# Kernel optimization log

Hardware: AMD Instinct MI355X
Metric: run time of the kernel (lower is better)

## Reference

```python
import jax, jax.numpy as jnp
import numpy as np

B, T, C, H, W, NC = 128, 32, 512, 8, 32, 6625
HH = C // 2  # per-direction LSTM hidden


def setup_inputs() -> dict:
    key = jax.random.key(0)
    ks = jax.random.split(key, 20)
    u = lambda k, shape, n: jax.random.uniform(k, shape, jnp.float32, -1.0 / np.sqrt(n), 1.0 / np.sqrt(n))
    return dict(
        feature=jax.random.normal(ks[0], (B, C, H, W), jnp.float32),
        attention_map=jax.random.uniform(ks[1], (B, T, H, W), jnp.float32) + 1e-3,
        text=jax.random.randint(ks[2], (B, T), 0, NC),
        text_length=jnp.full((B,), T, dtype=jnp.int32),
        char_embeddings=jax.random.normal(ks[3], (NC, C), jnp.float32),
        lstm_w_ih_f=u(ks[4], (4 * HH, C), HH),
        lstm_w_hh_f=u(ks[5], (4 * HH, HH), HH),
        lstm_b_ih_f=u(ks[6], (4 * HH,), HH),
        lstm_b_hh_f=u(ks[7], (4 * HH,), HH),
        lstm_w_ih_b=u(ks[8], (4 * HH, C), HH),
        lstm_w_hh_b=u(ks[9], (4 * HH, HH), HH),
        lstm_b_ih_b=u(ks[10], (4 * HH,), HH),
        lstm_b_hh_b=u(ks[11], (4 * HH,), HH),
        gru_w_ih=u(ks[12], (3 * C, 2 * C), C),
        gru_w_hh=u(ks[13], (3 * C, C), C),
        gru_b_ih=u(ks[14], (3 * C,), C),
        gru_b_hh=u(ks[15], (3 * C,), C),
        gen_w=u(ks[16], (NC, C), C),
        gen_b=u(ks[17], (NC,), C),
    )


def _lstm_dir(xs, w_ih, w_hh, b_ih, b_hh):
    # xs: [T, B, C] -> hs: [T, B, HH]; PyTorch gate order i, f, g, o
    b = xs.shape[1]
    hh = w_hh.shape[1]
    def step(carry, xt):
        h, c = carry
        g = xt @ w_ih.T + h @ w_hh.T + (b_ih + b_hh)
        i, f, gg, o = jnp.split(g, 4, axis=-1)
        c = jax.nn.sigmoid(f) * c + jax.nn.sigmoid(i) * jnp.tanh(gg)
        h = jax.nn.sigmoid(o) * jnp.tanh(c)
        return (h, c), h
    h0 = jnp.zeros((b, hh), xs.dtype)
    _, hs = jax.lax.scan(step, (h0, h0), xs)
    return hs


def reference(feature, attention_map, text, text_length, char_embeddings,
              lstm_w_ih_f, lstm_w_hh_f, lstm_b_ih_f, lstm_b_hh_f,
              lstm_w_ih_b, lstm_w_hh_b, lstm_b_ih_b, lstm_b_hh_b,
              gru_w_ih, gru_w_hh, gru_b_ih, gru_b_hh, gen_w, gen_b):
    b, c, h, w = feature.shape
    t = attention_map.shape[1]
    # normalize attention over spatial dims, attention-pool features: [T, B, C]
    att = attention_map / attention_map.sum(axis=(2, 3), keepdims=True)
    cseq = jnp.einsum('bchw,bthw->tbc', feature, att)
    # bidirectional LSTM (dropout is identity in eval mode)
    hs_f = _lstm_dir(cseq, lstm_w_ih_f, lstm_w_hh_f, lstm_b_ih_f, lstm_b_hh_f)
    hs_b = _lstm_dir(cseq[::-1], lstm_w_ih_b, lstm_w_hh_b, lstm_b_ih_b, lstm_b_hh_b)[::-1]
    cseq = jnp.concatenate([hs_f, hs_b], axis=-1)  # [T, B, C]
    # teacher-forced previous-char embeddings: step 0 uses index 0
    prev_idx = jnp.concatenate([jnp.zeros((b, 1), text.dtype), text[:, :-1]], axis=1)  # [B, T]
    prev_emb = jnp.transpose(char_embeddings[prev_idx], (1, 0, 2))  # [T, B, C]
    # GRUCell decode; PyTorch gate order r, z, n
    def gru_step(hid, inp):
        ct, pe = inp
        x = jnp.concatenate([ct, pe], axis=-1)  # [B, 2C]
        gi = x @ gru_w_ih.T + gru_b_ih
        gh = hid @ gru_w_hh.T + gru_b_hh
        ir, iz, inn = jnp.split(gi, 3, axis=-1)
        hr, hz, hn = jnp.split(gh, 3, axis=-1)
        r = jax.nn.sigmoid(ir + hr)
        z = jax.nn.sigmoid(iz + hz)
        n = jnp.tanh(inn + r * hn)
        hid = (1.0 - z) * n + z * hid
        return hid, hid
    h0 = jnp.zeros((b, c), cseq.dtype)
    _, gru_res = jax.lax.scan(gru_step, h0, (cseq, prev_emb))  # [T, B, C]
    logits = gru_res @ gen_w.T + gen_b  # [T, B, NC]
    # pack per text_length; lengths are all == T so this equals a reshape
    out_res = jnp.transpose(logits, (1, 0, 2)).reshape(b * t, -1)
    out_attentions = att.reshape(b * t, h, w)
    return (out_res, out_attentions)
```

## Files before the change

### kernel.cpp

```cpp
#include <hip/hip_runtime.h>
#include <math.h>

typedef __attribute__((ext_vector_type(8))) short sh8;
typedef __attribute__((ext_vector_type(4))) short sh4;
typedef __attribute__((ext_vector_type(4))) float f4;
typedef __attribute__((ext_vector_type(4))) unsigned u4;

__device__ inline short f2bf(float f) {
    union { float f; unsigned u; } v; v.f = f;
    unsigned u = v.u;
    return (short)((u + 0x7fffu + ((u >> 16) & 1u)) >> 16);
}
__device__ inline sh8 as_sh8(u4 v) { union { u4 u; sh8 s; } c; c.u = v; return c.s; }

__device__ inline float sigm(float x)  { return __builtin_amdgcn_rcpf(1.f + __builtin_amdgcn_exp2f(-1.44269504f * x)); }
__device__ inline float tanha(float x) { return 1.f - 2.f * __builtin_amdgcn_rcpf(1.f + __builtin_amdgcn_exp2f(2.88539008f * x)); }

__device__ inline sh8 frag8(const float* __restrict__ p) {
    f4 a = *(const f4*)p;
    f4 b = *(const f4*)(p + 4);
    sh8 r;
    r[0]=f2bf(a[0]); r[1]=f2bf(a[1]); r[2]=f2bf(a[2]); r[3]=f2bf(a[3]);
    r[4]=f2bf(b[0]); r[5]=f2bf(b[1]); r[6]=f2bf(b[2]); r[7]=f2bf(b[3]);
    return r;
}

__device__ inline u4 cload_u4(const void* p) {
    u4 r;
    asm volatile("global_load_dwordx4 %0, %1, off sc0 sc1" : "=v"(r) : "v"(p));
    return r;
}

__device__ inline void grp_signal(int* myflag, int epoch) {
    asm volatile("s_waitcnt vmcnt(0)" ::: "memory");
    __builtin_amdgcn_sched_barrier(0);
    __syncthreads();
    if (threadIdx.x == 0)
        __hip_atomic_store(myflag, epoch, __ATOMIC_RELAXED, __HIP_MEMORY_SCOPE_AGENT);
}
__device__ inline void grp_wait(const int* fbase, int nb, int epoch) {
    if (threadIdx.x < 64) {
        int lane = threadIdx.x;
        bool need = lane < nb;
        const int* fp = fbase + lane * 16;
        while (true) {
            int v = need ? __hip_atomic_load(fp, __ATOMIC_RELAXED, __HIP_MEMORY_SCOPE_AGENT)
                         : 0x7fffffff;
            if (__ballot(need && (v < epoch)) == 0ull) break;
            __builtin_amdgcn_s_sleep(1);
        }
    }
    __syncthreads();
}
__device__ inline void prefetch_drain() {
    asm volatile("s_waitcnt vmcnt(0)" ::: "memory");
    __builtin_amdgcn_sched_barrier(0);
}

__global__ void zero_ctr(int* c, int n) {
    int i = blockIdx.x * blockDim.x + threadIdx.x;
    if (i < n) c[i] = 0;
}

struct CvtPack { const float* s[7]; short* d[7]; int n4[7]; };
__global__ void cvt_bf16(CvtPack p) {
    int job = blockIdx.y;
    const f4* s = (const f4*)p.s[job];
    sh4* d = (sh4*)p.d[job];
    int n4 = p.n4[job];
    for (int i = blockIdx.x * blockDim.x + threadIdx.x; i < n4; i += gridDim.x * blockDim.x) {
        f4 v = s[i];
        sh4 o; o[0]=f2bf(v[0]); o[1]=f2bf(v[1]); o[2]=f2bf(v[2]); o[3]=f2bf(v[3]);
        d[i] = o;
    }
}

__global__ void bias_prep(const float* bihf, const float* bhhf,
                          const float* bihb, const float* bhhb, float* biasL) {
    int n = blockIdx.x * blockDim.x + threadIdx.x;
    biasL[n] = (n < 1024) ? bihf[n] + bhhf[n] : bihb[n - 1024] + bhhb[n - 1024];
}

__global__ void att_norm(const float* __restrict__ att, float* __restrict__ outA) {
    int row = blockIdx.x;
    int tid = threadIdx.x;
    const float* p = att + (size_t)row * 256;
    f4 v = *(const f4*)(p + tid * 4);
    float sum = v[0] + v[1] + v[2] + v[3];
    #pragma unroll
    for (int off = 32; off; off >>= 1) sum += __shfl_down(sum, off);
    float inv = 1.f / __shfl(sum, 0);
    f4 o; o[0]=v[0]*inv; o[1]=v[1]*inv; o[2]=v[2]*inv; o[3]=v[3]*inv;
    *(f4*)(outA + (size_t)row * 256 + tid * 4) = o;
}

__global__ __launch_bounds__(256)
void pool_gemm(const float* __restrict__ feature, const float* __restrict__ att,
               short* __restrict__ cseqb) {
    int bz = blockIdx.y;
    const float* A  = feature + (size_t)bz * 512 * 256;
    const float* Wt = att + (size_t)bz * 32 * 256;
    int wave = threadIdx.x >> 6, lane = threadIdx.x & 63, r = lane & 15, hh = lane >> 4;
    int m0 = blockIdx.x * 64 + wave * 16;
    f4 acc[2] = {};
    const float* ar = A  + (size_t)(m0 + r) * 256 + hh * 8;
    const float* w0 = Wt + (size_t)r * 256 + hh * 8;
    const float* w1 = Wt + (size_t)(16 + r) * 256 + hh * 8;
    for (int kk = 0; kk < 256; kk += 32) {
        sh8 af = frag8(ar + kk);
        acc[0] = __builtin_amdgcn_mfma_f32_16x16x32_bf16(af, frag8(w0 + kk), acc[0], 0, 0, 0);
        acc[1] = __builtin_amdgcn_mfma_f32_16x16x32_bf16(af, frag8(w1 + kk), acc[1], 0, 0, 0);
    }
    #pragma unroll
    for (int j = 0; j < 2; j++) {
        int t = j * 16 + r;
        #pragma unroll
        for (int reg = 0; reg < 4; reg++) {
            int c = m0 + hh * 4 + reg;
            cseqb[(size_t)t * 65536 + (size_t)bz * 512 + c] = f2bf(acc[j][reg]);
        }
    }
}

template<int MODE>
__global__ __launch_bounds__(256)
void gemm128(const short* __restrict__ A, const short* __restrict__ W,
             const float* __restrict__ bias1, const float* __restrict__ bias2,
             float* __restrict__ out, int M, int N, int K) {
    __shared__ short lds[2][2][4096];
    const int tid = threadIdx.x, wave = tid >> 6, lane = tid & 63;
    const int r = lane & 15, hh = lane >> 4;
    const int wm = wave >> 1, wn = wave & 1;

    int bx = blockIdx.x, by = blockIdx.y;
    {
        int gx = gridDim.x;
        int nwg = gx * gridDim.y;
        if ((nwg & 7) == 0) {
            int id = by * gx + bx;
            int cpx = nwg >> 3;
            int swz = (id & 7) * cpx + (id >> 3);
            bx = swz % gx;
            by = swz / gx;
        }
    }
    const int m0 = bx * 128, n0 = by * 128;

    const int c0 = tid, c1 = 256 + tid;
    const int r0 = c0 >> 2, r1 = c1 >> 2;
    const int s0 = ((c0 & 3) ^ ((r0 >> 1) & 3));
    const int s1 = ((c1 & 3) ^ ((r1 >> 1) & 3));
    const short* gA0 = A + (size_t)(m0 + r0) * K + s0 * 8;
    const short* gA1 = A + (size_t)(m0 + r1) * K + s1 * 8;
    int wr0 = n0 + r0; if (wr0 > N - 1) wr0 = N - 1;
    int wr1 = n0 + r1; if (wr1 > N - 1) wr1 = N - 1;
    const short* gW0 = W + (size_t)wr0 * K + s0 * 8;
    const short* gW1 = W + (size_t)wr1 * K + s1 * 8;
    const int lo0 = (wave * 64) * 8, lo1 = (256 + wave * 64) * 8;

    auto stage = [&](int buf, int kt) {
        int ko = kt * 32;
        __builtin_amdgcn_global_load_lds((const __attribute__((address_space(1))) void*)(gA0 + ko),
            (__attribute__((address_space(3))) void*)&lds[buf][0][lo0], 16, 0, 0);
        __builtin_amdgcn_global_load_lds((const __attribute__((address_space(1))) void*)(gA1 + ko),
            (__attribute__((address_space(3))) void*)&lds[buf][0][lo1], 16, 0, 0);
        __builtin_amdgcn_global_load_lds((const __attribute__((address_space(1))) void*)(gW0 + ko),
            (__attribute__((address_space(3))) void*)&lds[buf][1][lo0], 16, 0, 0);
        __builtin_amdgcn_global_load_lds((const __attribute__((address_space(1))) void*)(gW1 + ko),
            (__attribute__((address_space(3))) void*)&lds[buf][1][lo1], 16, 0, 0);
    };

    f4 acc[4][4] = {};
    const int NT = K / 32;
    int cur = 0;

    stage(0, 0);
    __syncthreads();
    for (int kt = 0; kt < NT; ++kt) {
        if (kt + 1 < NT) stage(cur ^ 1, kt + 1);
        const char* As = (const char*)&lds[cur][0][0];
        const char* Ws = (const char*)&lds[cur][1][0];
        sh8 a[4], b[4];
        #pragma unroll
        for (int i = 0; i < 4; i++) {
            int row = wm * 64 + i * 16 + r;
            a[i] = *(const sh8*)(As + row * 64 + ((hh ^ ((row >> 1) & 3)) * 16));
        }
        #pragma unroll
        for (int i = 0; i < 4; i++) {
            int row = wn * 64 + i * 16 + r;
            b[i] = *(const sh8*)(Ws + row * 64 + ((hh ^ ((row >> 1) & 3)) * 16));
        }
        #pragma unroll
        for (int i = 0; i < 4; i++)
            #pragma unroll
            for (int j = 0; j < 4; j++)
                acc[i][j] = __builtin_amdgcn_mfma_f32_16x16x32_bf16(a[i], b[j], acc[i][j], 0, 0, 0);
        __syncthreads();
        cur ^= 1;
    }

    float bsj[4];
    #pragma unroll
    for (int j = 0; j < 4; j++) {
        int n = n0 + wn * 64 + j * 16 + r;
        int nc = n < N ? n : N - 1;
        bsj[j] = (bias1 ? bias1[nc] : 0.f) + (bias2 ? bias2[nc] : 0.f);
    }

    float* fl = (float*)&lds[0][0][0];
    #pragma unroll
    for (int hhalf = 0; hhalf < 2; hhalf++) {
        __syncthreads();
        if (wm == hhalf) {
            #pragma unroll
            for (int i = 0; i < 4; i++)
                #pragma unroll
                for (int j = 0; j < 4; j++) {
                    int col = wn * 64 + j * 16 + r;
                    #pragma unroll
                    for (int reg = 0; reg < 4; reg++)
                        fl[(i * 16 + hh * 4 + reg) * 128 + col] = acc[i][j][reg] + bsj[j];
                }
        }
        __syncthreads();
        #pragma unroll
        for (int it = 0; it < 8; it++) {
            int c = it * 256 + tid;
            int row = c >> 5, cf4 = c & 31;
            int n = n0 + cf4 * 4;
            int mrow = m0 + hhalf * 64 + row;
            size_t orow = (MODE == 0) ? (size_t)mrow
                                      : ((size_t)(mrow & 127) * 32 + (mrow >> 7));
            if (n + 3 < N) {
                *(f4*)&out[orow * N + n] = *(const f4*)&fl[row * 128 + cf4 * 4];
            } else {
                #pragma unroll
                for (int d = 0; d < 4; d++)
                    if (n + d < N) out[orow * N + n + d] = fl[row * 128 + cf4 * 4 + d];
            }
        }
    }
}

__global__ void emb_fill(const int* __restrict__ text, const float* __restrict__ emb,
                         short* __restrict__ xcatb) {
    int n = blockIdx.x;
    int t = n >> 7, b = n & 127;
    int idx = (t == 0) ? 0 : text[b * 32 + (t - 1)];
    const f4* src = (const f4*)(emb + (size_t)idx * 512);
    sh4* dst = (sh4*)(xcatb + (size_t)n * 1024 + 512);
    for (int j = threadIdx.x; j < 128; j += 64) {
        f4 v = src[j];
        sh4 o; o[0]=f2bf(v[0]); o[1]=f2bf(v[1]); o[2]=f2bf(v[2]); o[3]=f2bf(v[3]);
        dst[j] = o;
    }
}

__global__ __launch_bounds__(128)
void lstm_chain(const float* __restrict__ xfb,
                const short* __restrict__ whhf_b, const short* __restrict__ whhb_b,
                short* __restrict__ xcatb,
                int* __restrict__ flags) {
    __shared__ short wlds[64 * 256];
    const int blk = blockIdx.x;
    const int dir = blk >> 6;
    const int mg  = (blk >> 4) & 3;
    const int ug  = blk & 15;
    const int m0 = mg * 32, u0 = ug * 16;
    const short* whh = dir ? whhb_b : whhf_b;
    const int dcol = dir ? 256 : 0;

    int* grp_flags = flags + (dir * 4 + mg) * 16 * 16;
    int* my_flag   = grp_flags + ug * 16;

    const int tid = threadIdx.x, mt = tid >> 6, lane = tid & 63;
    const int r = lane & 15, hh = lane >> 4;
    unsigned* xcat32 = (unsigned*)xcatb;

    for (int i = 0; i < 16; i++) {
        int c = i * 128 + tid;
        int col = c >> 5, off = c & 31;
        int g = col >> 4, ul = col & 15;
        sh8 v = *(const sh8*)(whh + ((size_t)(g * 256 + u0 + ul)) * 256 + off * 8);
        *(sh8*)((char*)wlds + col * 512 + ((off * 16) ^ ((col & 7) << 4))) = v;
    }
    __syncthreads();

    const int arow_m = m0 + mt * 16 + r;
    const int u = u0 + r;
    const int mb = m0 + mt * 16 + hh * 4;
    float c_state[4] = {0.f, 0.f, 0.f, 0.f};

    float xv[4][4];
    {
        const int t0 = dir ? 31 : 0;
        #pragma unroll
        for (int g = 0; g < 4; g++)
            #pragma unroll
            for (int reg = 0; reg < 4; reg++)
                xv[g][reg] = xfb[((size_t)t0 * 128 + mb + reg) * 2048 + dir * 1024 + g * 256 + u];
    }

    for (int s = 0; s < 32; s++) {
        const int t = dir ? (31 - s) : s;
        f4 acc[4] = {};
        if (s > 0) {
            grp_wait(grp_flags, 16, s);
            const int tp = dir ? (t + 1) : (t - 1);
            const short* arow = xcatb + ((size_t)tp * 128 + arow_m) * 1024 + dcol + hh * 8;
            u4 afr[8];
            #pragma unroll
            for (int kk = 0; kk < 8; kk++) afr[kk] = cload_u4(arow + kk * 32);
            asm volatile("s_waitcnt vmcnt(0)" ::: "memory");
            __builtin_amdgcn_sched_barrier(0);
            #pragma unroll
            for (int kk = 0; kk < 8; kk++) {
                sh8 af = as_sh8(afr[kk]);
                #pragma unroll
                for (int g = 0; g < 4; g++) {
                    int colr = g * 16 + r;
                    sh8 bf = *(const sh8*)((const char*)wlds + colr * 512 +
                              (((kk * 64 + hh * 16)) ^ ((colr & 7) << 4)));
                    acc[g] = __builtin_amdgcn_mfma_f32_16x16x32_bf16(af, bf, acc[g], 0, 0, 0);
                }
            }
        }
        #pragma unroll
        for (int reg = 0; reg < 4; reg++) {
            int m = mb + reg;
            float gI = acc[0][reg] + xv[0][reg];
            float gF = acc[1][reg] + xv[1][reg];
            float gG = acc[2][reg] + xv[2][reg];
            float gO = acc[3][reg] + xv[3][reg];
            float cn = sigm(gF) * c_state[reg] + sigm(gI) * tanha(gG);
            c_state[reg] = cn;
            float h = sigm(gO) * tanha(cn);
            unsigned hb = (unsigned)(unsigned short)f2bf(h);
            unsigned pb = (unsigned)__shfl_xor((int)hb, 1, 64);
            if (!(r & 1))
                __hip_atomic_store(&xcat32[((size_t)t * 128 + m) * 512 + ((dcol + u) >> 1)],
                                   hb | (pb << 16), __ATOMIC_RELAXED, __HIP_MEMORY_SCOPE_AGENT);
        }
        if (s < 31) {
            grp_signal(my_flag, s + 1);
            const int tn = dir ? (t - 1) : (t + 1);
            #pragma unroll
            for (int g = 0; g < 4; g++)
                #pragma unroll
                for (int reg = 0; reg < 4; reg++)
                    xv[g][reg] = xfb[((size_t)tn * 128 + mb + reg) * 2048 + dir * 1024 + g * 256 + u];
            prefetch_drain();
        }
    }
}

__global__ __launch_bounds__(128)
void gru_chain(const float* __restrict__ gi,
               const short* __restrict__ gwhh_b, const float* __restrict__ bhh,
               short* __restrict__ gresb,
               int* __restrict__ flags) {
    extern __shared__ short wlds[];
    const int blk = blockIdx.x;
    const int mg = blk >> 4, ug = blk & 15;
    const int m0 = mg * 16, u0 = ug * 32;

    int* grp_flags = flags + mg * 16 * 16;
    int* my_flag   = grp_flags + ug * 16;

    const int tid = threadIdx.x, w = tid >> 6, lane = tid & 63;
    const int r = lane & 15, hh = lane >> 4;
    unsigned* gres32 = (unsigned*)gresb;

    for (int i = 0; i < 48; i++) {
        int c = i * 128 + tid;
        int col = c >> 6, off = c & 63;
        int g = col >> 5, ul = col & 31;
        sh8 v = *(const sh8*)(gwhh_b + ((size_t)(g * 512 + u0 + ul)) * 512 + off * 8);
        *(sh8*)((char*)wlds + col * 1024 + ((off * 16) ^ ((col & 7) << 4))) = v;
    }
    __syncthreads();

    const int mb = m0 + hh * 4;
    const int u = u0 + w * 16 + r;
    const float bh_r = bhh[u], bh_z = bhh[512 + u], bh_n = bhh[1024 + u];
    float h_state[4] = {0.f, 0.f, 0.f, 0.f};

    float gv[3][4];
    #pragma unroll
    for (int g = 0; g < 3; g++)
        #pragma unroll
        for (int reg = 0; reg < 4; reg++)
            gv[g][reg] = gi[((size_t)(mb + reg)) * 1536 + g * 512 + u];

    for (int t = 0; t < 32; t++) {
        f4 acc[3] = {};
        if (t > 0) {
            grp_wait(grp_flags, 16, t);
            const short* arow = gresb + ((size_t)(t - 1) * 128 + m0 + r) * 512 + hh * 8;
            u4 afr[16];
            #pragma unroll
            for (int kk = 0; kk < 16; kk++) afr[kk] = cload_u4(arow + kk * 32);
            asm volatile("s_waitcnt vmcnt(0)" ::: "memory");
            __builtin_amdgcn_sched_barrier(0);
            #pragma unroll
            for (int kk = 0; kk < 16; kk++) {
                sh8 af = as_sh8(afr[kk]);
                #pragma unroll
                for (int g = 0; g < 3; g++) {
                    int colr = g * 32 + w * 16 + r;
                    sh8 bf = *(const sh8*)((const char*)wlds + colr * 1024 +
                              ((kk * 64 + hh * 16) ^ ((colr & 7) << 4)));
                    acc[g] = __builtin_amdgcn_mfma_f32_16x16x32_bf16(af, bf, acc[g], 0, 0, 0);
                }
            }
        }
        #pragma unroll
        for (int reg = 0; reg < 4; reg++) {
            int m = mb + reg;
            float rr = sigm(gv[0][reg] + acc[0][reg] + bh_r);
            float zz = sigm(gv[1][reg] + acc[1][reg] + bh_z);
            float nn = tanha(gv[2][reg] + rr * (acc[2][reg] + bh_n));
            float h = (1.f - zz) * nn + zz * h_state[reg];
            h_state[reg] = h;
            unsigned hb = (unsigned)(unsigned short)f2bf(h);
            unsigned pb = (unsigned)__shfl_xor((int)hb, 1, 64);
            if (!(r & 1))
                __hip_atomic_store(&gres32[((size_t)t * 128 + m) * 256 + (u >> 1)],
                                   hb | (pb << 16), __ATOMIC_RELAXED, __HIP_MEMORY_SCOPE_AGENT);
        }
        if (t < 31) {
            grp_signal(my_flag, t + 1);
            #pragma unroll
            for (int g = 0; g < 3; g++)
                #pragma unroll
                for (int reg = 0; reg < 4; reg++)
                    gv[g][reg] = gi[((size_t)(t + 1) * 128 + mb + reg) * 1536 + g * 512 + u];
            prefetch_drain();
        }
    }
}

extern "C" void kernel_launch(void* const* d_in, const int* in_sizes, int n_in,
                              void* d_out, int out_size, void* d_ws, size_t ws_size,
                              hipStream_t stream) {
    const float* feature = (const float*)d_in[0];
    const float* attmap  = (const float*)d_in[1];
    const int*   text    = (const int*)d_in[2];
    const float* cemb    = (const float*)d_in[4];
    const float* wihf    = (const float*)d_in[5];
    const float* whhf    = (const float*)d_in[6];
    const float* bihf    = (const float*)d_in[7];
    const float* bhhf    = (const float*)d_in[8];
    const float* wihb    = (const float*)d_in[9];
    const float* whhb    = (const float*)d_in[10];
    const float* bihb    = (const float*)d_in[11];
    const float* bhhb    = (const float*)d_in[12];
    const float* gwih    = (const float*)d_in[13];
    const float* gwhh    = (const float*)d_in[14];
    const float* gbih    = (const float*)d_in[15];
    const float* gbhh    = (const float*)d_in[16];
    const float* genw    = (const float*)d_in[17];
    const float* genb    = (const float*)d_in[18];

    float* out    = (float*)d_out;
    float* outAtt = out + (size_t)4096 * 6625;

    float* xfb   = (float*)d_ws;
    float* gi    = xfb + 8388608;
    float* biasL = gi + 6291456;
    int*   flags = (int*)(biasL + 2048);
    short* cseqb  = (short*)(flags + 4096);
    short* xcatb  = cseqb + 2097152;
    short* gresb  = xcatb + 4194304;
    short* wih_b  = gresb + 2097152;
    short* whhf_b = wih_b + 1048576;
    short* whhb_b = whhf_b + 262144;
    short* gwih_b = whhb_b + 262144;
    short* gwhh_b = gwih_b + 1572864;
    short* genw_b = gwhh_b + 786432;

    hipFuncSetAttribute((const void*)gru_chain,
                        hipFuncAttributeMaxDynamicSharedMemorySize, 98304);

    zero_ctr<<<dim3(16), dim3(256), 0, stream>>>(flags, 4096);

    CvtPack p;
    p.s[0] = wihf; p.d[0] = wih_b;           p.n4[0] = 524288 / 4;
    p.s[1] = wihb; p.d[1] = wih_b + 524288;  p.n4[1] = 524288 / 4;
    p.s[2] = whhf; p.d[2] = whhf_b;          p.n4[2] = 262144 / 4;
    p.s[3] = whhb; p.d[3] = whhb_b;          p.n4[3] = 262144 / 4;
    p.s[4] = gwih; p.d[4] = gwih_b;          p.n4[4] = 1572864 / 4;
    p.s[5] = gwhh; p.d[5] = gwhh_b;          p.n4[5] = 786432 / 4;
    p.s[6] = genw; p.d[6] = genw_b;          p.n4[6] = 3392000 / 4;
    cvt_bf16<<<dim3(128, 7), dim3(256), 0, stream>>>(p);
    bias_prep<<<dim3(8), dim3(256), 0, stream>>>(bihf, bhhf, bihb, bhhb, biasL);

    att_norm<<<dim3(4096), dim3(64), 0, stream>>>(attmap, outAtt);
    pool_gemm<<<dim3(8, 128), dim3(256), 0, stream>>>(feature, outAtt, cseqb);

    gemm128<0><<<dim3(32, 16), dim3(256), 0, stream>>>(cseqb, wih_b, biasL, nullptr,
                                                       xfb, 4096, 2048, 512);
    emb_fill<<<dim3(4096), dim3(64), 0, stream>>>(text, cemb, xcatb);

    lstm_chain<<<dim3(128), dim3(128), 0, stream>>>(xfb, whhf_b, whhb_b, xcatb, flags);

    gemm128<0><<<dim3(32, 12), dim3(256), 0, stream>>>(xcatb, gwih_b, gbih, nullptr,
                                                       gi, 4096, 1536, 1024);

    gru_chain<<<dim3(128), dim3(128), 98304, stream>>>(gi, gwhh_b, gbhh, gresb, flags + 2048);

    gemm128<1><<<dim3(32, 52), dim3(256), 0, stream>>>(gresb, genw_b, genb, nullptr,
                                                       out, 4096, 6625, 512);
}
```

Baseline: 385.0 us.

## Add 256x128 GEMM tile for generator projection and fuse prep kernels

Adds a new gemm256 kernel with 512 threads and a 256-row M tile for the final vocabulary projection. It stages A and W tiles into LDS with direct global-to-LDS loads and double buffering, so each loaded W tile is reused across twice as many rows. The zero-counter and bias-prep kernels are merged into one launch to remove a kernel launch. The cost is higher LDS and register pressure per workgroup and only 832 workgroups for the large GEMM.

```diff
diff --git a/kernel.cpp b/kernel.cpp
--- a/kernel.cpp
+++ b/kernel.cpp
@@ -57,9 +57,12 @@
     __builtin_amdgcn_sched_barrier(0);
 }
 
-__global__ void zero_ctr(int* c, int n) {
+__global__ void prep(int* flags, const float* bihf, const float* bhhf,
+                     const float* bihb, const float* bhhb, float* biasL) {
     int i = blockIdx.x * blockDim.x + threadIdx.x;
-    if (i < n) c[i] = 0;
+    flags[i] = 0;
+    if (i < 2048)
+        biasL[i] = (i < 1024) ? bihf[i] + bhhf[i] : bihb[i - 1024] + bhhb[i - 1024];
 }
 
 struct CvtPack { const float* s[7]; short* d[7]; int n4[7]; };
@@ -73,12 +76,6 @@
         sh4 o; o[0]=f2bf(v[0]); o[1]=f2bf(v[1]); o[2]=f2bf(v[2]); o[3]=f2bf(v[3]);
         d[i] = o;
     }
-}
-
-__global__ void bias_prep(const float* bihf, const float* bhhf,
-                          const float* bihb, const float* bhhb, float* biasL) {
-    int n = blockIdx.x * blockDim.x + threadIdx.x;
-    biasL[n] = (n < 1024) ? bihf[n] + bhhf[n] : bihb[n - 1024] + bhhb[n - 1024];
 }
 
 __global__ void att_norm(const float* __restrict__ att, float* __restrict__ outA) {
@@ -122,7 +119,6 @@
     }
 }
 
-template<int MODE>
 __global__ __launch_bounds__(256)
 void gemm128(const short* __restrict__ A, const short* __restrict__ W,
              const float* __restrict__ bias1, const float* __restrict__ bias2,
@@ -230,8 +226,123 @@
             int row = c >> 5, cf4 = c & 31;
             int n = n0 + cf4 * 4;
             int mrow = m0 + hhalf * 64 + row;
-            size_t orow = (MODE == 0) ? (size_t)mrow
-                                      : ((size_t)(mrow & 127) * 32 + (mrow >> 7));
+            if (n + 3 < N) {
+                *(f4*)&out[(size_t)mrow * N + n] = *(const f4*)&fl[row * 128 + cf4 * 4];
+            } else {
+                #pragma unroll
+                for (int d = 0; d < 4; d++)
+                    if (n + d < N) out[(size_t)mrow * N + n + d] = fl[row * 128 + cf4 * 4 + d];
+            }
+        }
+    }
+}
+
+__global__ __launch_bounds__(512)
+void gemm256(const short* __restrict__ A, const short* __restrict__ W,
+             const float* __restrict__ bias1,
+             float* __restrict__ out, int M, int N, int K) {
+    __shared__ short lds[2][12288];
+    const int tid = threadIdx.x, wave = tid >> 6, lane = tid & 63;
+    const int r = lane & 15, hh = lane >> 4;
+    const int wm = wave >> 1, wn = wave & 1;
+
+    int bx = blockIdx.x, by = blockIdx.y;
+    {
+        int gx = gridDim.x;
+        int nwg = gx * gridDim.y;
+        if ((nwg & 7) == 0) {
+            int id = by * gx + bx;
+            int cpx = nwg >> 3;
+            int swz = (id & 7) * cpx + (id >> 3);
+            bx = swz % gx;
+            by = swz / gx;
+        }
+    }
+    const int m0 = bx * 256, n0 = by * 128;
+
+    const int cA0 = tid, cA1 = 512 + tid, cW = tid;
+    const int rA0 = cA0 >> 2, rA1 = cA1 >> 2, rW = cW >> 2;
+    const int sA0 = (cA0 & 3) ^ ((rA0 >> 1) & 3);
+    const int sA1 = (cA1 & 3) ^ ((rA1 >> 1) & 3);
+    const int sW  = (cW & 3) ^ ((rW >> 1) & 3);
+    const short* gA0 = A + (size_t)(m0 + rA0) * K + sA0 * 8;
+    const short* gA1 = A + (size_t)(m0 + rA1) * K + sA1 * 8;
+    int wrW = n0 + rW; if (wrW > N - 1) wrW = N - 1;
+    const short* gW0 = W + (size_t)wrW * K + sW * 8;
+    const int loA0 = (wave * 64) * 8, loA1 = (512 + wave * 64) * 8;
+    const int loW  = 8192 + (wave * 64) * 8;
+
+    auto stage = [&](int buf, int kt) {
+        int ko = kt * 32;
+        __builtin_amdgcn_global_load_lds((const __attribute__((address_space(1))) void*)(gA0 + ko),
+            (__attribute__((address_space(3))) void*)&lds[buf][loA0], 16, 0, 0);
+        __builtin_amdgcn_global_load_lds((const __attribute__((address_space(1))) void*)(gA1 + ko),
+            (__attribute__((address_space(3))) void*)&lds[buf][loA1], 16, 0, 0);
+        __builtin_amdgcn_global_load_lds((const __attribute__((address_space(1))) void*)(gW0 + ko),
+            (__attribute__((address_space(3))) void*)&lds[buf][loW], 16, 0, 0);
+    };
+
+    f4 acc[4][4] = {};
+    const int NT = K / 32;
+    int cur = 0;
+
+    stage(0, 0);
+    __syncthreads();
+    for (int kt = 0; kt < NT; ++kt) {
+        if (kt + 1 < NT) stage(cur ^ 1, kt + 1);
+        const char* As = (const char*)&lds[cur][0];
+        const char* Ws = (const char*)&lds[cur][8192];
+        sh8 a[4], b[4];
+        #pragma unroll
+        for (int i = 0; i < 4; i++) {
+            int row = wm * 64 + i * 16 + r;
+            a[i] = *(const sh8*)(As + row * 64 + ((hh ^ ((row >> 1) & 3)) * 16));
+        }
+        #pragma unroll
+        for (int i = 0; i < 4; i++) {
+            int row = wn * 64 + i * 16 + r;
+            b[i] = *(const sh8*)(Ws + row * 64 + ((hh ^ ((row >> 1) & 3)) * 16));
+        }
+        #pragma unroll
+        for (int i = 0; i < 4; i++)
+            #pragma unroll
+            for (int j = 0; j < 4; j++)
+                acc[i][j] = __builtin_amdgcn_mfma_f32_16x16x32_bf16(a[i], b[j], acc[i][j], 0, 0, 0);
+        __syncthreads();
+        cur ^= 1;
+    }
+
+    float bsj[4];
+    #pragma unroll
+    for (int j = 0; j < 4; j++) {
+        int n = n0 + wn * 64 + j * 16 + r;
+        int nc = n < N ? n : N - 1;
+        bsj[j] = bias1 ? bias1[nc] : 0.f;
+    }
+
+    float* fl = (float*)&lds[0][0];
+    #pragma unroll
+    for (int q = 0; q < 4; q++) {
+        __syncthreads();
+        if (wm == q) {
+            #pragma unroll
+            for (int i = 0; i < 4; i++)
+                #pragma unroll
+                for (int j = 0; j < 4; j++) {
+                    int col = wn * 64 + j * 16 + r;
+                    #pragma unroll
+                    for (int reg = 0; reg < 4; reg++)
+                        fl[(i * 16 + hh * 4 + reg) * 128 + col] = acc[i][j][reg] + bsj[j];
+                }
+        }
+        __syncthreads();
+        #pragma unroll
+        for (int it = 0; it < 4; it++) {
+            int c = it * 512 + tid;
+            int row = c >> 5, cf4 = c & 31;
+            int n = n0 + cf4 * 4;
+            int mrow = m0 + q * 64 + row;
+            size_t orow = (size_t)(mrow & 127) * 32 + (mrow >> 7);
             if (n + 3 < N) {
                 *(f4*)&out[orow * N + n] = *(const f4*)&fl[row * 128 + cf4 * 4];
             } else {
@@ -483,7 +594,7 @@
     hipFuncSetAttribute((const void*)gru_chain,
                         hipFuncAttributeMaxDynamicSharedMemorySize, 98304);
 
-    zero_ctr<<<dim3(16), dim3(256), 0, stream>>>(flags, 4096);
+    prep<<<dim3(16), dim3(256), 0, stream>>>(flags, bihf, bhhf, bihb, bhhb, biasL);
 
     CvtPack p;
     p.s[0] = wihf; p.d[0] = wih_b;           p.n4[0] = 524288 / 4;
@@ -494,22 +605,21 @@
     p.s[5] = gwhh; p.d[5] = gwhh_b;          p.n4[5] = 786432 / 4;
     p.s[6] = genw; p.d[6] = genw_b;          p.n4[6] = 3392000 / 4;
     cvt_bf16<<<dim3(128, 7), dim3(256), 0, stream>>>(p);
-    bias_prep<<<dim3(8), dim3(256), 0, stream>>>(bihf, bhhf, bihb, bhhb, biasL);
 
     att_norm<<<dim3(4096), dim3(64), 0, stream>>>(attmap, outAtt);
     pool_gemm<<<dim3(8, 128), dim3(256), 0, stream>>>(feature, outAtt, cseqb);
 
-    gemm128<0><<<dim3(32, 16), dim3(256), 0, stream>>>(cseqb, wih_b, biasL, nullptr,
-                                                       xfb, 4096, 2048, 512);
+    gemm128<<<dim3(32, 16), dim3(256), 0, stream>>>(cseqb, wih_b, biasL, nullptr,
+                                                    xfb, 4096, 2048, 512);
     emb_fill<<<dim3(4096), dim3(64), 0, stream>>>(text, cemb, xcatb);
 
     lstm_chain<<<dim3(128), dim3(128), 0, stream>>>(xfb, whhf_b, whhb_b, xcatb, flags);
 
-    gemm128<0><<<dim3(32, 12), dim3(256), 0, stream>>>(xcatb, gwih_b, gbih, nullptr,
-                                                       gi, 4096, 1536, 1024);
+    gemm128<<<dim3(32, 12), dim3(256), 0, stream>>>(xcatb, gwih_b, gbih, nullptr,
+                                                    gi, 4096, 1536, 1024);
 
     gru_chain<<<dim3(128), dim3(128), 98304, stream>>>(gi, gwhh_b, gbhh, gresb, flags + 2048);
 
-    gemm128<1><<<dim3(32, 52), dim3(256), 0, stream>>>(gresb, genw_b, genb, nullptr,
-                                                       out, 4096, 6625, 512);
-}
+    gemm256<<<dim3(16, 52), dim3(512), 0, stream>>>(gresb, genw_b, genb,
+                                                    out, 4096, 6625, 512);
+}
```

After: 375.2 us. -2.5%, faster.

## Enlarge GEMM tile to 256x128 with 8 waves and fold bias prep into flag init

Applied to the files above, without the earlier changes.

The bf16 MFMA GEMM moves from 128x128 tiles with 4 waves to 256x128 tiles with 8 waves. Each block now stages 256 A rows and 128 W rows per k-step, so the W tile is reused across twice as many rows and fewer blocks are launched. The epilogue writes through LDS in four 64-row quarters. Separately, the bias-sum kernel is merged into the flag-zeroing kernel to save one launch. In exchange, blocks are larger and fewer, which lowers the block count for the smaller GEMMs (192 to 256 blocks), and LDS use per block rises.

```diff
diff --git a/kernel.cpp b/kernel.cpp
--- a/kernel.cpp
+++ b/kernel.cpp
@@ -57,9 +57,12 @@
     __builtin_amdgcn_sched_barrier(0);
 }
 
-__global__ void zero_ctr(int* c, int n) {
+__global__ void prep(int* flags, const float* bihf, const float* bhhf,
+                     const float* bihb, const float* bhhb, float* biasL) {
     int i = blockIdx.x * blockDim.x + threadIdx.x;
-    if (i < n) c[i] = 0;
+    flags[i] = 0;
+    if (i < 2048)
+        biasL[i] = (i < 1024) ? bihf[i] + bhhf[i] : bihb[i - 1024] + bhhb[i - 1024];
 }
 
 struct CvtPack { const float* s[7]; short* d[7]; int n4[7]; };
@@ -73,12 +76,6 @@
         sh4 o; o[0]=f2bf(v[0]); o[1]=f2bf(v[1]); o[2]=f2bf(v[2]); o[3]=f2bf(v[3]);
         d[i] = o;
     }
-}
-
-__global__ void bias_prep(const float* bihf, const float* bhhf,
-                          const float* bihb, const float* bhhb, float* biasL) {
-    int n = blockIdx.x * blockDim.x + threadIdx.x;
-    biasL[n] = (n < 1024) ? bihf[n] + bhhf[n] : bihb[n - 1024] + bhhb[n - 1024];
 }
 
 __global__ void att_norm(const float* __restrict__ att, float* __restrict__ outA) {
@@ -123,11 +120,11 @@
 }
 
 template<int MODE>
-__global__ __launch_bounds__(256)
-void gemm128(const short* __restrict__ A, const short* __restrict__ W,
-             const float* __restrict__ bias1, const float* __restrict__ bias2,
+__global__ __launch_bounds__(512)
+void gemm256(const short* __restrict__ A, const short* __restrict__ W,
+             const float* __restrict__ bias1,
              float* __restrict__ out, int M, int N, int K) {
-    __shared__ short lds[2][2][4096];
+    __shared__ short lds[2][12288];
     const int tid = threadIdx.x, wave = tid >> 6, lane = tid & 63;
     const int r = lane & 15, hh = lane >> 4;
     const int wm = wave >> 1, wn = wave & 1;
@@ -144,30 +141,28 @@
             by = swz / gx;
         }
     }
-    const int m0 = bx * 128, n0 = by * 128;
-
-    const int c0 = tid, c1 = 256 + tid;
-    const int r0 = c0 >> 2, r1 = c1 >> 2;
-    const int s0 = ((c0 & 3) ^ ((r0 >> 1) & 3));
-    const int s1 = ((c1 & 3) ^ ((r1 >> 1) & 3));
-    const short* gA0 = A + (size_t)(m0 + r0) * K + s0 * 8;
-    const short* gA1 = A + (size_t)(m0 + r1) * K + s1 * 8;
-    int wr0 = n0 + r0; if (wr0 > N - 1) wr0 = N - 1;
-    int wr1 = n0 + r1; if (wr1 > N - 1) wr1 = N - 1;
-    const short* gW0 = W + (size_t)wr0 * K + s0 * 8;
-    const short* gW1 = W + (size_t)wr1 * K + s1 * 8;
-    const int lo0 = (wave * 64) * 8, lo1 = (256 + wave * 64) * 8;
+    const int m0 = bx * 256, n0 = by * 128;
+
+    const int cA0 = tid, cA1 = 512 + tid, cW = tid;
+    const int rA0 = cA0 >> 2, rA1 = cA1 >> 2, rW = cW >> 2;
+    const int sA0 = (cA0 & 3) ^ ((rA0 >> 1) & 3);
+    const int sA1 = (cA1 & 3) ^ ((rA1 >> 1) & 3);
+    const int sW  = (cW & 3) ^ ((rW >> 1) & 3);
+    const short* gA0 = A + (size_t)(m0 + rA0) * K + sA0 * 8;
+    const short* gA1 = A + (size_t)(m0 + rA1) * K + sA1 * 8;
+    int wrW = n0 + rW; if (wrW > N - 1) wrW = N - 1;
+    const short* gW0 = W + (size_t)wrW * K + sW * 8;
+    const int loA0 = (wave * 64) * 8, loA1 = (512 + wave * 64) * 8;
+    const int loW  = 8192 + (wave * 64) * 8;
 
     auto stage = [&](int buf, int kt) {
         int ko = kt * 32;
         __builtin_amdgcn_global_load_lds((const __attribute__((address_space(1))) void*)(gA0 + ko),
-            (__attribute__((address_space(3))) void*)&lds[buf][0][lo0], 16, 0, 0);
+            (__attribute__((address_space(3))) void*)&lds[buf][loA0], 16, 0, 0);
         __builtin_amdgcn_global_load_lds((const __attribute__((address_space(1))) void*)(gA1 + ko),
-            (__attribute__((address_space(3))) void*)&lds[buf][0][lo1], 16, 0, 0);
+            (__attribute__((address_space(3))) void*)&lds[buf][loA1], 16, 0, 0);
         __builtin_amdgcn_global_load_lds((const __attribute__((address_space(1))) void*)(gW0 + ko),
-            (__attribute__((address_space(3))) void*)&lds[buf][1][lo0], 16, 0, 0);
-        __builtin_amdgcn_global_load_lds((const __attribute__((address_space(1))) void*)(gW1 + ko),
-            (__attribute__((address_space(3))) void*)&lds[buf][1][lo1], 16, 0, 0);
+            (__attribute__((address_space(3))) void*)&lds[buf][loW], 16, 0, 0);
     };
 
     f4 acc[4][4] = {};
@@ -178,8 +173,8 @@
     __syncthreads();
     for (int kt = 0; kt < NT; ++kt) {
         if (kt + 1 < NT) stage(cur ^ 1, kt + 1);
-        const char* As = (const char*)&lds[cur][0][0];
-        const char* Ws = (const char*)&lds[cur][1][0];
+        const char* As = (const char*)&lds[cur][0];
+        const char* Ws = (const char*)&lds[cur][8192];
         sh8 a[4], b[4];
         #pragma unroll
         for (int i = 0; i < 4; i++) {
@@ -205,14 +200,14 @@
     for (int j = 0; j < 4; j++) {
         int n = n0 + wn * 64 + j * 16 + r;
         int nc = n < N ? n : N - 1;
-        bsj[j] = (bias1 ? bias1[nc] : 0.f) + (bias2 ? bias2[nc] : 0.f);
-    }
-
-    float* fl = (float*)&lds[0][0][0];
+        bsj[j] = bias1 ? bias1[nc] : 0.f;
+    }
+
+    float* fl = (float*)&lds[0][0];
     #pragma unroll
-    for (int hhalf = 0; hhalf < 2; hhalf++) {
+    for (int q = 0; q < 4; q++) {
         __syncthreads();
-        if (wm == hhalf) {
+        if (wm == q) {
             #pragma unroll
             for (int i = 0; i < 4; i++)
                 #pragma unroll
@@ -225,11 +220,11 @@
         }
         __syncthreads();
         #pragma unroll
-        for (int it = 0; it < 8; it++) {
-            int c = it * 256 + tid;
+        for (int it = 0; it < 4; it++) {
+            int c = it * 512 + tid;
             int row = c >> 5, cf4 = c & 31;
             int n = n0 + cf4 * 4;
-            int mrow = m0 + hhalf * 64 + row;
+            int mrow = m0 + q * 64 + row;
             size_t orow = (MODE == 0) ? (size_t)mrow
                                       : ((size_t)(mrow & 127) * 32 + (mrow >> 7));
             if (n + 3 < N) {
@@ -483,7 +478,7 @@
     hipFuncSetAttribute((const void*)gru_chain,
                         hipFuncAttributeMaxDynamicSharedMemorySize, 98304);
 
-    zero_ctr<<<dim3(16), dim3(256), 0, stream>>>(flags, 4096);
+    prep<<<dim3(16), dim3(256), 0, stream>>>(flags, bihf, bhhf, bihb, bhhb, biasL);
 
     CvtPack p;
     p.s[0] = wihf; p.d[0] = wih_b;           p.n4[0] = 524288 / 4;
@@ -494,22 +489,21 @@
     p.s[5] = gwhh; p.d[5] = gwhh_b;          p.n4[5] = 786432 / 4;
     p.s[6] = genw; p.d[6] = genw_b;          p.n4[6] = 3392000 / 4;
     cvt_bf16<<<dim3(128, 7), dim3(256), 0, stream>>>(p);
-    bias_prep<<<dim3(8), dim3(256), 0, stream>>>(bihf, bhhf, bihb, bhhb, biasL);
 
     att_norm<<<dim3(4096), dim3(64), 0, stream>>>(attmap, outAtt);
     pool_gemm<<<dim3(8, 128), dim3(256), 0, stream>>>(feature, outAtt, cseqb);
 
-    gemm128<0><<<dim3(32, 16), dim3(256), 0, stream>>>(cseqb, wih_b, biasL, nullptr,
+    gemm256<0><<<dim3(16, 16), dim3(512), 0, stream>>>(cseqb, wih_b, biasL,
                                                        xfb, 4096, 2048, 512);
     emb_fill<<<dim3(4096), dim3(64), 0, stream>>>(text, cemb, xcatb);
 
     lstm_chain<<<dim3(128), dim3(128), 0, stream>>>(xfb, whhf_b, whhb_b, xcatb, flags);
 
-    gemm128<0><<<dim3(32, 12), dim3(256), 0, stream>>>(xcatb, gwih_b, gbih, nullptr,
+    gemm256<0><<<dim3(16, 12), dim3(512), 0, stream>>>(xcatb, gwih_b, gbih,
                                                        gi, 4096, 1536, 1024);
 
     gru_chain<<<dim3(128), dim3(128), 98304, stream>>>(gi, gwhh_b, gbhh, gresb, flags + 2048);
 
-    gemm128<1><<<dim3(32, 52), dim3(256), 0, stream>>>(gresb, genw_b, genb, nullptr,
+    gemm256<1><<<dim3(16, 52), dim3(512), 0, stream>>>(gresb, genw_b, genb,
                                                        out, 4096, 6625, 512);
 }
```

Measured after the change: 381.0 us. No clear change (-1.0%).
